# Kernel tuning notes

Measured on AMD Instinct MI355X. Metric: run time of the kernel, lower is better.

The kernel has to match this reference:

```python
import jax, jax.numpy as jnp
import numpy as np

NODELEN = 394
N_NODES = 50000
N_EDGES = 200000
IN_DIM = 2 * NODELEN  # 788
H2 = 192
EMB = 128


def setup_inputs() -> dict:
    key = jax.random.key(0)
    ks = jax.random.split(key, 12)
    inp = {
        'features': jax.random.normal(ks[0], (N_NODES, NODELEN), dtype=jnp.float32),
        'src': jax.random.randint(ks[1], (N_EDGES,), 0, N_NODES),
        'dst': jax.random.randint(ks[2], (N_EDGES,), 0, N_NODES),
        # AutoEncoder params (Linear weights stored as [in, out])
        'W_enc1': jax.random.normal(ks[3], (IN_DIM, H2), dtype=jnp.float32) / np.sqrt(IN_DIM),
        'b_enc1': jnp.zeros((H2,), dtype=jnp.float32),
        'W_enc3': jax.random.normal(ks[4], (H2, EMB), dtype=jnp.float32) / np.sqrt(H2),
        'b_enc3': jnp.zeros((EMB,), dtype=jnp.float32),
        'W_dec1': jax.random.normal(ks[5], (EMB, H2), dtype=jnp.float32) / np.sqrt(EMB),
        'b_dec1': jnp.zeros((H2,), dtype=jnp.float32),
        'W_dec3': jax.random.normal(ks[6], (H2, IN_DIM), dtype=jnp.float32) / np.sqrt(H2),
        'b_dec3': jnp.zeros((IN_DIM,), dtype=jnp.float32),
    }
    return inp


def _segment_mean(msgs, dst, inv_deg, n):
    # msgs: [E, F] gathered neighbor features; mean over incoming edges per node
    return jax.ops.segment_sum(msgs, dst, num_segments=n) * inv_deg


def reference(features, src, dst, W_enc1, b_enc1, W_enc3, b_enc3,
              W_dec1, b_dec1, W_dec3, b_dec3):
    n = features.shape[0]
    ones = jnp.ones(src.shape[0], dtype=features.dtype)
    deg = jax.ops.segment_sum(ones, dst, num_segments=n)
    # nodes with no neighbors fall back to the zero dummy vector (as in source)
    inv_deg = (1.0 / jnp.maximum(deg, 1.0))[:, None]

    # depth-1 aggregation: mean of raw neighbor features, then feat[0] := 0
    h1 = _segment_mean(features[src], dst, inv_deg, n)
    h1 = h1.at[:, 0].set(0.0)
    # depth-2 aggregation: mean of depth-1 aggregates of neighbors, feat[0] := 0
    h2 = _segment_mean(h1[src], dst, inv_deg, n)
    h2 = h2.at[:, 0].set(0.0)

    # concatenated embedding with positions 0 and NODELEN zeroed
    emb = jnp.concatenate([features, h2], axis=1)  # [N, 788]
    emb = emb.at[:, 0].set(0.0).at[:, NODELEN].set(0.0)

    # AutoEncoder forward (dropout is identity at inference)
    x = jax.nn.relu(emb @ W_enc1 + b_enc1)
    encoded = x @ W_enc3 + b_enc3
    y = jax.nn.relu(encoded @ W_dec1 + b_dec1)
    decoded = y @ W_dec3 + b_dec3
    return encoded, decoded, emb
```

## Files before the change

### kernel.cpp

```cpp
#include <hip/hip_runtime.h>
#include <hip/hip_bf16.h>

#define NODELEN 394
#define IN_DIM 788
#define H2DIM 192
#define EMBDIM 128
#define NCHUNK 197

typedef __attribute__((ext_vector_type(4))) float f32x4;
typedef __attribute__((ext_vector_type(8))) short bfrag;

static __device__ __forceinline__ unsigned short f2bf(float f) {
    union { float f; unsigned u; } v; v.f = f;
    unsigned r = v.u + 0x7FFFu + ((v.u >> 16) & 1u);
    return (unsigned short)(r >> 16);
}
static __device__ __forceinline__ float bf2f(unsigned short h) {
    union { unsigned u; float f; } v; v.u = ((unsigned)h) << 16;
    return v.f;
}


__global__ void count_deg(const int* __restrict__ dst, int* __restrict__ deg, int e) {
    int i = blockIdx.x * blockDim.x + threadIdx.x;
    if (i < e) atomicAdd(&deg[dst[i]], 1);
}

__global__ void block_sum(const int* __restrict__ deg, int* __restrict__ bsum, int n) {
    __shared__ int s[256];
    int t = threadIdx.x;
    int i = blockIdx.x * 256 + t;
    s[t] = (i < n) ? deg[i] : 0;
    __syncthreads();
    for (int d = 128; d > 0; d >>= 1) {
        if (t < d) s[t] += s[t + d];
        __syncthreads();
    }
    if (t == 0) bsum[blockIdx.x] = s[0];
}

__global__ void scan_bsums(int* bsum, int nb) {
    __shared__ int s[256];
    int t = threadIdx.x;
    int x0 = (t < nb) ? bsum[t] : 0;
    s[t] = x0;
    __syncthreads();
    for (int d = 1; d < 256; d <<= 1) {
        int u = (t >= d) ? s[t - d] : 0;
        __syncthreads();
        s[t] += u;
        __syncthreads();
    }
    if (t < nb) bsum[t] = s[t] - x0;
}

__global__ void block_scan(const int* __restrict__ deg, const int* __restrict__ boff,
                           int* __restrict__ rowstart, int* __restrict__ cursor,
                           float* __restrict__ inv, int n) {
    __shared__ int s[256];
    int t = threadIdx.x;
    int i = blockIdx.x * 256 + t;
    int x0 = (i < n) ? deg[i] : 0;
    s[t] = x0;
    __syncthreads();
    for (int d = 1; d < 256; d <<= 1) {
        int u = (t >= d) ? s[t - d] : 0;
        __syncthreads();
        s[t] += u;
        __syncthreads();
    }
    if (i < n) {
        int r = boff[blockIdx.x] + s[t] - x0;
        rowstart[i] = r;
        cursor[i] = r;
        inv[i] = 1.0f / fmaxf((float)x0, 1.0f);
    }
}

__global__ void fill_edges(const int* __restrict__ src, const int* __restrict__ dst,
                           int* __restrict__ cursor, int* __restrict__ elist, int e) {
    int i = blockIdx.x * blockDim.x + threadIdx.x;
    if (i < e) {
        int p = atomicAdd(&cursor[dst[i]], 1);
        elist[p] = src[i];
    }
}


__global__ __launch_bounds__(256) void gather1(
        const float* __restrict__ feat, const int* __restrict__ rowstart,
        const int* __restrict__ deg, const float* __restrict__ inv,
        const int* __restrict__ elist, unsigned short* __restrict__ h1) {
    const int node = blockIdx.x;
    const int c = threadIdx.x;
    if (c >= NCHUNK) return;
    const int beg = rowstart[node];
    const int dc = deg[node];
    const float s = inv[node];
    const size_t off = (size_t)c * 2;

    float ax = 0.f, ay = 0.f, bx = 0.f, by = 0.f;
    float cx = 0.f, cy = 0.f, dx = 0.f, dy = 0.f;
    int j = 0;
    for (; j + 3 < dc; j += 4) {
        int n0 = elist[beg + j], n1 = elist[beg + j + 1];
        int n2 = elist[beg + j + 2], n3 = elist[beg + j + 3];
        float2 v0 = *(const float2*)(feat + (size_t)n0 * NODELEN + off);
        float2 v1 = *(const float2*)(feat + (size_t)n1 * NODELEN + off);
        float2 v2 = *(const float2*)(feat + (size_t)n2 * NODELEN + off);
        float2 v3 = *(const float2*)(feat + (size_t)n3 * NODELEN + off);
        ax += v0.x; ay += v0.y; bx += v1.x; by += v1.y;
        cx += v2.x; cy += v2.y; dx += v3.x; dy += v3.y;
    }
    for (; j < dc; ++j) {
        int n0 = elist[beg + j];
        float2 v0 = *(const float2*)(feat + (size_t)n0 * NODELEN + off);
        ax += v0.x; ay += v0.y;
    }
    float fx = (ax + bx + cx + dx) * s;
    float fy = (ay + by + cy + dy) * s;
    if (c == 0) fx = 0.f;
    unsigned out = ((unsigned)f2bf(fy) << 16) | (unsigned)f2bf(fx);
    *(unsigned*)(h1 + (size_t)node * NODELEN + off) = out;
}

__global__ __launch_bounds__(256) void gather2_emb(
        const float* __restrict__ feat, const unsigned* __restrict__ h1,
        const int* __restrict__ rowstart, const int* __restrict__ deg,
        const float* __restrict__ inv, const int* __restrict__ elist,
        float* __restrict__ emb) {
    const int node = blockIdx.x;
    const int c = threadIdx.x;
    if (c >= NCHUNK) return;
    const int beg = rowstart[node];
    const int dc = deg[node];
    const float s = inv[node];

    float ax = 0.f, ay = 0.f, bx = 0.f, by = 0.f;
    float cx = 0.f, cy = 0.f, dx = 0.f, dy = 0.f;
    int j = 0;
    for (; j + 3 < dc; j += 4) {
        int n0 = elist[beg + j], n1 = elist[beg + j + 1];
        int n2 = elist[beg + j + 2], n3 = elist[beg + j + 3];
        unsigned u0 = h1[(size_t)n0 * NCHUNK + c];
        unsigned u1 = h1[(size_t)n1 * NCHUNK + c];
        unsigned u2 = h1[(size_t)n2 * NCHUNK + c];
        unsigned u3 = h1[(size_t)n3 * NCHUNK + c];
        ax += bf2f((unsigned short)u0); ay += bf2f((unsigned short)(u0 >> 16));
        bx += bf2f((unsigned short)u1); by += bf2f((unsigned short)(u1 >> 16));
        cx += bf2f((unsigned short)u2); cy += bf2f((unsigned short)(u2 >> 16));
        dx += bf2f((unsigned short)u3); dy += bf2f((unsigned short)(u3 >> 16));
    }
    for (; j < dc; ++j) {
        int n0 = elist[beg + j];
        unsigned u0 = h1[(size_t)n0 * NCHUNK + c];
        ax += bf2f((unsigned short)u0); ay += bf2f((unsigned short)(u0 >> 16));
    }
    float hx = (ax + bx + cx + dx) * s;
    float hy = (ay + by + cy + dy) * s;

    const float* fr = feat + (size_t)node * NODELEN;
    float* er = emb + (size_t)node * IN_DIM;
    float2 fv = *(const float2*)(fr + c * 2);
    if (c == 0) { fv.x = 0.f; hx = 0.f; }
    *(float2*)(er + c * 2) = fv;
    float2 hv; hv.x = hx; hv.y = hy;
    *(float2*)(er + NODELEN + c * 2) = hv;
}

__device__ __forceinline__ void tr_one(const float* W, unsigned short* Wt,
                                       int K, int N, int Kp, int idx) {
    int nrow = idx / Kp, k = idx - nrow * Kp;
    Wt[idx] = (k < K) ? f2bf(W[(size_t)k * N + nrow]) : (unsigned short)0;
}

#define T1E (192 * 800)
#define T2E (128 * 192)
#define T3E (192 * 128)
#define T4E (788 * 192)

__global__ void transpose_all(const float* __restrict__ W1, unsigned short* __restrict__ Wt1,
                              const float* __restrict__ W2, unsigned short* __restrict__ Wt2,
                              const float* __restrict__ W3, unsigned short* __restrict__ Wt3,
                              const float* __restrict__ W4, unsigned short* __restrict__ Wt4) {
    int idx = blockIdx.x * 256 + threadIdx.x;
    if (idx < T1E) { tr_one(W1, Wt1, IN_DIM, H2DIM, 800, idx); return; }
    idx -= T1E;
    if (idx < T2E) { tr_one(W2, Wt2, H2DIM, EMBDIM, 192, idx); return; }
    idx -= T2E;
    if (idx < T3E) { tr_one(W3, Wt3, EMBDIM, H2DIM, 128, idx); return; }
    idx -= T3E;
    if (idx < T4E) { tr_one(W4, Wt4, H2DIM, IN_DIM, 192, idx); return; }
}

__global__ __launch_bounds__(256) void mlp_fused(
    const float* __restrict__ emb,
    const unsigned short* __restrict__ Wt1,
    const unsigned short* __restrict__ Wt2,
    const unsigned short* __restrict__ Wt3,
    const unsigned short* __restrict__ Wt4,
    const float* __restrict__ b1, const float* __restrict__ b2,
    const float* __restrict__ b3, const float* __restrict__ b4,
    float* __restrict__ encoded, float* __restrict__ decoded, int M)
{
    __shared__ unsigned short As[64][40];
    __shared__ unsigned short Bs[192][40];
    __shared__ unsigned short XY[64][200];
    __shared__ unsigned short EN[64][136];

    const int tid = threadIdx.x;
    const int wid = tid >> 6, l = tid & 63;
    const int wm = wid >> 1, wn = wid & 1;
    const int lr = l & 15, lk = l >> 4;
    const int m0 = blockIdx.x * 64;

    {
        f32x4 acc[2][6];
        #pragma unroll
        for (int i = 0; i < 2; ++i)
            #pragma unroll
            for (int j = 0; j < 6; ++j) acc[i][j] = (f32x4){0.f, 0.f, 0.f, 0.f};

        for (int kt = 0; kt < 25; ++kt) {
            const int k0 = kt * 32;
            {
                int row = tid >> 2, q = tid & 3;
                int gm = m0 + row, gk = k0 + q * 8;
                float4 v0 = make_float4(0.f, 0.f, 0.f, 0.f);
                float4 v1 = make_float4(0.f, 0.f, 0.f, 0.f);
                if (gm < M) {
                    if (gk < IN_DIM)     v0 = *(const float4*)(emb + (size_t)gm * IN_DIM + gk);
                    if (gk + 4 < IN_DIM) v1 = *(const float4*)(emb + (size_t)gm * IN_DIM + gk + 4);
                }
                union { unsigned short u[8]; bfrag v; } pk;
                pk.u[0] = f2bf(v0.x); pk.u[1] = f2bf(v0.y);
                pk.u[2] = f2bf(v0.z); pk.u[3] = f2bf(v0.w);
                pk.u[4] = f2bf(v1.x); pk.u[5] = f2bf(v1.y);
                pk.u[6] = f2bf(v1.z); pk.u[7] = f2bf(v1.w);
                *(bfrag*)&As[row][q * 8] = pk.v;
            }
            for (int a = tid; a < 384; a += 256) {
                int row = a >> 1, h = a & 1;
                const unsigned short* p = Wt1 + (size_t)row * 800 + k0 + h * 16;
                *(bfrag*)&Bs[row][h * 16]     = *(const bfrag*)p;
                *(bfrag*)&Bs[row][h * 16 + 8] = *(const bfrag*)(p + 8);
            }
            __syncthreads();
            bfrag af[2], bf[6];
            #pragma unroll
            for (int i = 0; i < 2; ++i) af[i] = *(const bfrag*)&As[wm * 32 + i * 16 + lr][lk * 8];
            #pragma unroll
            for (int j = 0; j < 6; ++j) bf[j] = *(const bfrag*)&Bs[wn * 96 + j * 16 + lr][lk * 8];
            #pragma unroll
            for (int i = 0; i < 2; ++i)
                #pragma unroll
                for (int j = 0; j < 6; ++j)
                    acc[i][j] = __builtin_amdgcn_mfma_f32_16x16x32_bf16(af[i], bf[j], acc[i][j], 0, 0, 0);
            __syncthreads();
        }
        float bv[6];
        #pragma unroll
        for (int j = 0; j < 6; ++j) bv[j] = b1[wn * 96 + j * 16 + lr];
        #pragma unroll
        for (int i = 0; i < 2; ++i)
            #pragma unroll
            for (int j = 0; j < 6; ++j)
                #pragma unroll
                for (int r = 0; r < 4; ++r) {
                    int m = wm * 32 + i * 16 + lk * 4 + r;
                    int n1 = wn * 96 + j * 16 + lr;
                    XY[m][n1] = f2bf(fmaxf(acc[i][j][r] + bv[j], 0.f));
                }
        __syncthreads();
    }

    {
        f32x4 acc[2][4];
        #pragma unroll
        for (int i = 0; i < 2; ++i)
            #pragma unroll
            for (int j = 0; j < 4; ++j) acc[i][j] = (f32x4){0.f, 0.f, 0.f, 0.f};

        for (int kt = 0; kt < 6; ++kt) {
            const int k0 = kt * 32;
            {
                int row = tid >> 1, h = tid & 1;
                const unsigned short* p = Wt2 + (size_t)row * 192 + k0 + h * 16;
                *(bfrag*)&Bs[row][h * 16]     = *(const bfrag*)p;
                *(bfrag*)&Bs[row][h * 16 + 8] = *(const bfrag*)(p + 8);
            }
            __syncthreads();
            bfrag af[2], bf[4];
            #pragma unroll
            for (int i = 0; i < 2; ++i) af[i] = *(const bfrag*)&XY[wm * 32 + i * 16 + lr][k0 + lk * 8];
            #pragma unroll
            for (int j = 0; j < 4; ++j) bf[j] = *(const bfrag*)&Bs[wn * 64 + j * 16 + lr][lk * 8];
            #pragma unroll
            for (int i = 0; i < 2; ++i)
                #pragma unroll
                for (int j = 0; j < 4; ++j)
                    acc[i][j] = __builtin_amdgcn_mfma_f32_16x16x32_bf16(af[i], bf[j], acc[i][j], 0, 0, 0);
            __syncthreads();
        }
        float bv[4];
        #pragma unroll
        for (int j = 0; j < 4; ++j) bv[j] = b2[wn * 64 + j * 16 + lr];
        #pragma unroll
        for (int i = 0; i < 2; ++i)
            #pragma unroll
            for (int j = 0; j < 4; ++j)
                #pragma unroll
                for (int r = 0; r < 4; ++r) {
                    int m = wm * 32 + i * 16 + lk * 4 + r;
                    int n2 = wn * 64 + j * 16 + lr;
                    float v = acc[i][j][r] + bv[j];
                    int gm = m0 + m;
                    if (gm < M) encoded[(size_t)gm * EMBDIM + n2] = v;
                    EN[m][n2] = f2bf(v);
                }
        __syncthreads();
    }

    {
        f32x4 acc[2][6];
        #pragma unroll
        for (int i = 0; i < 2; ++i)
            #pragma unroll
            for (int j = 0; j < 6; ++j) acc[i][j] = (f32x4){0.f, 0.f, 0.f, 0.f};

        for (int kt = 0; kt < 4; ++kt) {
            const int k0 = kt * 32;
            for (int a = tid; a < 384; a += 256) {
                int row = a >> 1, h = a & 1;
                const unsigned short* p = Wt3 + (size_t)row * 128 + k0 + h * 16;
                *(bfrag*)&Bs[row][h * 16]     = *(const bfrag*)p;
                *(bfrag*)&Bs[row][h * 16 + 8] = *(const bfrag*)(p + 8);
            }
            __syncthreads();
            bfrag af[2], bf[6];
            #pragma unroll
            for (int i = 0; i < 2; ++i) af[i] = *(const bfrag*)&EN[wm * 32 + i * 16 + lr][k0 + lk * 8];
            #pragma unroll
            for (int j = 0; j < 6; ++j) bf[j] = *(const bfrag*)&Bs[wn * 96 + j * 16 + lr][lk * 8];
            #pragma unroll
            for (int i = 0; i < 2; ++i)
                #pragma unroll
                for (int j = 0; j < 6; ++j)
                    acc[i][j] = __builtin_amdgcn_mfma_f32_16x16x32_bf16(af[i], bf[j], acc[i][j], 0, 0, 0);
            __syncthreads();
        }
        float bv[6];
        #pragma unroll
        for (int j = 0; j < 6; ++j) bv[j] = b3[wn * 96 + j * 16 + lr];
        #pragma unroll
        for (int i = 0; i < 2; ++i)
            #pragma unroll
            for (int j = 0; j < 6; ++j)
                #pragma unroll
                for (int r = 0; r < 4; ++r) {
                    int m = wm * 32 + i * 16 + lk * 4 + r;
                    int n3 = wn * 96 + j * 16 + lr;
                    XY[m][n3] = f2bf(fmaxf(acc[i][j][r] + bv[j], 0.f));
                }
        __syncthreads();
    }

    for (int nc = 0; nc < 7; ++nc) {
        f32x4 acc[2][4];
        #pragma unroll
        for (int i = 0; i < 2; ++i)
            #pragma unroll
            for (int j = 0; j < 4; ++j) acc[i][j] = (f32x4){0.f, 0.f, 0.f, 0.f};

        for (int kt = 0; kt < 6; ++kt) {
            const int k0 = kt * 32;
            {
                int row = tid >> 1, h = tid & 1;
                int gn = nc * 128 + row;
                bfrag v0 = {0,0,0,0,0,0,0,0}, v1 = {0,0,0,0,0,0,0,0};
                if (gn < IN_DIM) {
                    const unsigned short* p = Wt4 + (size_t)gn * 192 + k0 + h * 16;
                    v0 = *(const bfrag*)p;
                    v1 = *(const bfrag*)(p + 8);
                }
                *(bfrag*)&Bs[row][h * 16]     = v0;
                *(bfrag*)&Bs[row][h * 16 + 8] = v1;
            }
            __syncthreads();
            bfrag af[2], bf[4];
            #pragma unroll
            for (int i = 0; i < 2; ++i) af[i] = *(const bfrag*)&XY[wm * 32 + i * 16 + lr][k0 + lk * 8];
            #pragma unroll
            for (int j = 0; j < 4; ++j) bf[j] = *(const bfrag*)&Bs[wn * 64 + j * 16 + lr][lk * 8];
            #pragma unroll
            for (int i = 0; i < 2; ++i)
                #pragma unroll
                for (int j = 0; j < 4; ++j)
                    acc[i][j] = __builtin_amdgcn_mfma_f32_16x16x32_bf16(af[i], bf[j], acc[i][j], 0, 0, 0);
            __syncthreads();
        }
        float bv[4];
        #pragma unroll
        for (int j = 0; j < 4; ++j) {
            int n4 = nc * 128 + wn * 64 + j * 16 + lr;
            bv[j] = (n4 < IN_DIM) ? b4[n4] : 0.f;
        }
        #pragma unroll
        for (int i = 0; i < 2; ++i)
            #pragma unroll
            for (int j = 0; j < 4; ++j)
                #pragma unroll
                for (int r = 0; r < 4; ++r) {
                    int m = wm * 32 + i * 16 + lk * 4 + r;
                    int n4 = nc * 128 + wn * 64 + j * 16 + lr;
                    int gm = m0 + m;
                    if (gm < M && n4 < IN_DIM)
                        decoded[(size_t)gm * IN_DIM + n4] = acc[i][j][r] + bv[j];
                }
    }
}


extern "C" void kernel_launch(void* const* d_in, const int* in_sizes, int n_in,
                              void* d_out, int out_size, void* d_ws, size_t ws_size,
                              hipStream_t stream) {
    const float* features = (const float*)d_in[0];
    const int*   src      = (const int*)d_in[1];
    const int*   dst      = (const int*)d_in[2];
    const float* W_enc1   = (const float*)d_in[3];
    const float* b_enc1   = (const float*)d_in[4];
    const float* W_enc3   = (const float*)d_in[5];
    const float* b_enc3   = (const float*)d_in[6];
    const float* W_dec1   = (const float*)d_in[7];
    const float* b_dec1   = (const float*)d_in[8];
    const float* W_dec3   = (const float*)d_in[9];
    const float* b_dec3   = (const float*)d_in[10];

    const int n = in_sizes[0] / NODELEN;
    const int e = in_sizes[1];

    float* encoded = (float*)d_out;
    float* decoded = encoded + (size_t)n * EMBDIM;
    float* emb     = decoded + (size_t)n * IN_DIM;

    char* ws = (char*)d_ws;
    unsigned short* h1  = (unsigned short*)(ws + 0);
    unsigned short* Wt1 = (unsigned short*)(ws + 40000000);
    unsigned short* Wt2 = (unsigned short*)(ws + 40400000);
    unsigned short* Wt3 = (unsigned short*)(ws + 40500000);
    unsigned short* Wt4 = (unsigned short*)(ws + 40600000);
    float* inv          = (float*)(ws + 41000000);
    int*   deg          = (int*)  (ws + 41200000);
    int*   rowstart     = (int*)  (ws + 41400000);
    int*   cursor       = (int*)  (ws + 41600000);
    int*   elist        = (int*)  (ws + 41800000);
    int*   bsum         = (int*)  (ws + 42600000);

    const int nb = (n + 255) / 256;
    const int eb = (e + 255) / 256;

    transpose_all<<<(T1E + T2E + T3E + T4E + 255) / 256, 256, 0, stream>>>(
        W_enc1, Wt1, W_enc3, Wt2, W_dec1, Wt3, W_dec3, Wt4);

    hipMemsetAsync(deg, 0, (size_t)n * sizeof(int), stream);
    count_deg<<<eb, 256, 0, stream>>>(dst, deg, e);
    block_sum<<<nb, 256, 0, stream>>>(deg, bsum, n);
    scan_bsums<<<1, 256, 0, stream>>>(bsum, nb);
    block_scan<<<nb, 256, 0, stream>>>(deg, bsum, rowstart, cursor, inv, n);
    fill_edges<<<eb, 256, 0, stream>>>(src, dst, cursor, elist, e);

    gather1<<<n, 256, 0, stream>>>(features, rowstart, deg, inv, elist, h1);
    gather2_emb<<<n, 256, 0, stream>>>(features, (const unsigned*)h1, rowstart, deg,
                                       inv, elist, emb);

    const int MB = (n + 63) / 64;
    mlp_fused<<<MB, 256, 0, stream>>>(emb, Wt1, Wt2, Wt3, Wt4,
                                      b_enc1, b_enc3, b_dec1, b_dec3,
                                      encoded, decoded, n);
}
```

Measured before the change: 387.7 us.

## Software-pipeline weight/activation loads in fused MLP and swizzle LDS layouts

Restructures the fused four-layer MLP kernel so global loads for the next K-tile (and the first tile of the next layer) are issued into registers while the current tile is consumed. The A operand of layer 1 is loaded straight into registers in MFMA fragment layout, which removes the As shared buffer. Padded LDS arrays become XOR-swizzled flat layouts to avoid bank conflicts, and the last layer caches its A fragments in registers across output chunks. It also switches to the library bf16 conversion and adds an occupancy hint. In exchange it uses more registers and more complex indexing, so spilling or lower occupancy are possible.

```diff
diff --git a/kernel.cpp b/kernel.cpp
--- a/kernel.cpp
+++ b/kernel.cpp
@@ -193,7 +193,58 @@
     if (idx < T4E) { tr_one(W4, Wt4, H2DIM, IN_DIM, 192, idx); return; }
 }
 
-__global__ __launch_bounds__(256) void mlp_fused(
+static __device__ __forceinline__ int bs_addr(int r, int s) {
+    return r * 32 + ((s ^ ((r >> 1) & 3)) << 3);
+}
+static __device__ __forceinline__ int xy_base(int r, int s) {
+    int ph = (s & 24) | ((s ^ r) & 7);
+    return r * 192 + (ph << 3);
+}
+static __device__ __forceinline__ int xy_addr_s(int r, int col) { return xy_base(r, col >> 3) + (col & 7); }
+static __device__ __forceinline__ int en_base(int r, int s) {
+    int ph = (s & 8) | ((s ^ r) & 7);
+    return r * 128 + (ph << 3);
+}
+static __device__ __forceinline__ int en_addr_s(int r, int col) { return en_base(r, col >> 3) + (col & 7); }
+
+static __device__ __forceinline__ unsigned short f2bf_fast(float f) {
+    __hip_bfloat16 h = __float2bfloat16(f);
+    union { __hip_bfloat16 h; unsigned short u; } c; c.h = h; return c.u;
+}
+
+struct A8 { float4 a, b; };
+
+static __device__ __forceinline__ void load_a(A8 out[2], const float* __restrict__ emb,
+                                              int m0, int wm, int lr, int lk, int M, int kt) {
+    int c = kt * 32 + lk * 8;
+    #pragma unroll
+    for (int i = 0; i < 2; ++i) {
+        int gm = m0 + wm * 32 + i * 16 + lr;
+        const float* rp = emb + (size_t)gm * IN_DIM;
+        bool v = gm < M;
+        if (v && c + 8 <= IN_DIM) {
+            out[i].a = *(const float4*)(rp + c);
+            out[i].b = *(const float4*)(rp + c + 4);
+        } else {
+            float t[8];
+            #pragma unroll
+            for (int q = 0; q < 8; ++q) t[q] = (v && c + q < IN_DIM) ? rp[c + q] : 0.f;
+            out[i].a = make_float4(t[0], t[1], t[2], t[3]);
+            out[i].b = make_float4(t[4], t[5], t[6], t[7]);
+        }
+    }
+}
+
+static __device__ __forceinline__ bfrag cvt_a(const A8& x) {
+    union { unsigned short u[8]; bfrag v; } pk;
+    pk.u[0] = f2bf_fast(x.a.x); pk.u[1] = f2bf_fast(x.a.y);
+    pk.u[2] = f2bf_fast(x.a.z); pk.u[3] = f2bf_fast(x.a.w);
+    pk.u[4] = f2bf_fast(x.b.x); pk.u[5] = f2bf_fast(x.b.y);
+    pk.u[6] = f2bf_fast(x.b.z); pk.u[7] = f2bf_fast(x.b.w);
+    return pk.v;
+}
+
+__global__ __launch_bounds__(256, 3) void mlp_fused(
     const float* __restrict__ emb,
     const unsigned short* __restrict__ Wt1,
     const unsigned short* __restrict__ Wt2,
@@ -203,61 +254,72 @@
     const float* __restrict__ b3, const float* __restrict__ b4,
     float* __restrict__ encoded, float* __restrict__ decoded, int M)
 {
-    __shared__ unsigned short As[64][40];
-    __shared__ unsigned short Bs[192][40];
-    __shared__ unsigned short XY[64][200];
-    __shared__ unsigned short EN[64][136];
+    __shared__ unsigned short Bs[192 * 32];
+    __shared__ unsigned short XY[64 * 192];
+    __shared__ unsigned short EN[64 * 128];
 
     const int tid = threadIdx.x;
     const int wid = tid >> 6, l = tid & 63;
     const int wm = wid >> 1, wn = wid & 1;
     const int lr = l & 15, lk = l >> 4;
     const int m0 = blockIdx.x * 64;
+    const bfrag zf = {0, 0, 0, 0, 0, 0, 0, 0};
+
+    const int r0 = tid >> 2, s0 = tid & 3;
+    const int r1 = (tid + 256) >> 2;
+    const int r2 = (tid + 512) >> 2;
+    const int bw0 = bs_addr(r0, s0);
+    const int bw1 = bs_addr(r1, s0);
+    const int bw2 = bs_addr(r2, s0);
+    int brd6[6], brd4[4];
+    #pragma unroll
+    for (int j = 0; j < 6; ++j) brd6[j] = bs_addr(wn * 96 + j * 16 + lr, lk);
+    #pragma unroll
+    for (int j = 0; j < 4; ++j) brd4[j] = bs_addr(wn * 64 + j * 16 + lr, lk);
 
     {
-        f32x4 acc[2][6];
+        f32x4 acc1[2][6];
         #pragma unroll
         for (int i = 0; i < 2; ++i)
             #pragma unroll
-            for (int j = 0; j < 6; ++j) acc[i][j] = (f32x4){0.f, 0.f, 0.f, 0.f};
-
+            for (int j = 0; j < 6; ++j) acc1[i][j] = (f32x4){0.f, 0.f, 0.f, 0.f};
+
+        A8 aC[2], aN[2];
+        bfrag bC[3], bN[3];
+        load_a(aC, emb, m0, wm, lr, lk, M, 0);
+        bC[0] = *(const bfrag*)(Wt1 + (size_t)r0 * 800 + s0 * 8);
+        bC[1] = *(const bfrag*)(Wt1 + (size_t)r1 * 800 + s0 * 8);
+        bC[2] = *(const bfrag*)(Wt1 + (size_t)r2 * 800 + s0 * 8);
+
+        #pragma unroll 5
         for (int kt = 0; kt < 25; ++kt) {
-            const int k0 = kt * 32;
-            {
-                int row = tid >> 2, q = tid & 3;
-                int gm = m0 + row, gk = k0 + q * 8;
-                float4 v0 = make_float4(0.f, 0.f, 0.f, 0.f);
-                float4 v1 = make_float4(0.f, 0.f, 0.f, 0.f);
-                if (gm < M) {
-                    if (gk < IN_DIM)     v0 = *(const float4*)(emb + (size_t)gm * IN_DIM + gk);
-                    if (gk + 4 < IN_DIM) v1 = *(const float4*)(emb + (size_t)gm * IN_DIM + gk + 4);
-                }
-                union { unsigned short u[8]; bfrag v; } pk;
-                pk.u[0] = f2bf(v0.x); pk.u[1] = f2bf(v0.y);
-                pk.u[2] = f2bf(v0.z); pk.u[3] = f2bf(v0.w);
-                pk.u[4] = f2bf(v1.x); pk.u[5] = f2bf(v1.y);
-                pk.u[6] = f2bf(v1.z); pk.u[7] = f2bf(v1.w);
-                *(bfrag*)&As[row][q * 8] = pk.v;
-            }
-            for (int a = tid; a < 384; a += 256) {
-                int row = a >> 1, h = a & 1;
-                const unsigned short* p = Wt1 + (size_t)row * 800 + k0 + h * 16;
-                *(bfrag*)&Bs[row][h * 16]     = *(const bfrag*)p;
-                *(bfrag*)&Bs[row][h * 16 + 8] = *(const bfrag*)(p + 8);
+            *(bfrag*)&Bs[bw0] = bC[0];
+            *(bfrag*)&Bs[bw1] = bC[1];
+            *(bfrag*)&Bs[bw2] = bC[2];
+            if (kt < 24) {
+                int k0 = (kt + 1) * 32;
+                load_a(aN, emb, m0, wm, lr, lk, M, kt + 1);
+                bN[0] = *(const bfrag*)(Wt1 + (size_t)r0 * 800 + k0 + s0 * 8);
+                bN[1] = *(const bfrag*)(Wt1 + (size_t)r1 * 800 + k0 + s0 * 8);
+                bN[2] = *(const bfrag*)(Wt1 + (size_t)r2 * 800 + k0 + s0 * 8);
             }
             __syncthreads();
-            bfrag af[2], bf[6];
-            #pragma unroll
-            for (int i = 0; i < 2; ++i) af[i] = *(const bfrag*)&As[wm * 32 + i * 16 + lr][lk * 8];
-            #pragma unroll
-            for (int j = 0; j < 6; ++j) bf[j] = *(const bfrag*)&Bs[wn * 96 + j * 16 + lr][lk * 8];
-            #pragma unroll
-            for (int i = 0; i < 2; ++i)
-                #pragma unroll
-                for (int j = 0; j < 6; ++j)
-                    acc[i][j] = __builtin_amdgcn_mfma_f32_16x16x32_bf16(af[i], bf[j], acc[i][j], 0, 0, 0);
+            bfrag af0 = cvt_a(aC[0]), af1 = cvt_a(aC[1]);
+            bfrag bf[6];
+            #pragma unroll
+            for (int j = 0; j < 6; ++j) bf[j] = *(const bfrag*)&Bs[brd6[j]];
+            #pragma unroll
+            for (int j = 0; j < 6; ++j) {
+                acc1[0][j] = __builtin_amdgcn_mfma_f32_16x16x32_bf16(af0, bf[j], acc1[0][j], 0, 0, 0);
+                acc1[1][j] = __builtin_amdgcn_mfma_f32_16x16x32_bf16(af1, bf[j], acc1[1][j], 0, 0, 0);
+            }
             __syncthreads();
+            if (kt < 24) {
+                aC[0] = aN[0]; aC[1] = aN[1];
+                bC[0] = bN[0]; bC[1] = bN[1]; bC[2] = bN[2];
+            }
         }
+
         float bv[6];
         #pragma unroll
         for (int j = 0; j < 6; ++j) bv[j] = b1[wn * 96 + j * 16 + lr];
@@ -269,39 +331,51 @@
                 for (int r = 0; r < 4; ++r) {
                     int m = wm * 32 + i * 16 + lk * 4 + r;
                     int n1 = wn * 96 + j * 16 + lr;
-                    XY[m][n1] = f2bf(fmaxf(acc[i][j][r] + bv[j], 0.f));
+                    XY[xy_addr_s(m, n1)] = f2bf_fast(fmaxf(acc1[i][j][r] + bv[j], 0.f));
                 }
-        __syncthreads();
-    }
-
+    }
+
+    bfrag c3[3], n3[3];
     {
-        f32x4 acc[2][4];
+        bfrag c2[2], n2[2];
+        c2[0] = *(const bfrag*)(Wt2 + (size_t)r0 * 192 + s0 * 8);
+        c2[1] = *(const bfrag*)(Wt2 + (size_t)r1 * 192 + s0 * 8);
+        f32x4 acc2[2][4];
         #pragma unroll
         for (int i = 0; i < 2; ++i)
             #pragma unroll
-            for (int j = 0; j < 4; ++j) acc[i][j] = (f32x4){0.f, 0.f, 0.f, 0.f};
-
+            for (int j = 0; j < 4; ++j) acc2[i][j] = (f32x4){0.f, 0.f, 0.f, 0.f};
+
+        #pragma unroll
         for (int kt = 0; kt < 6; ++kt) {
-            const int k0 = kt * 32;
-            {
-                int row = tid >> 1, h = tid & 1;
-                const unsigned short* p = Wt2 + (size_t)row * 192 + k0 + h * 16;
-                *(bfrag*)&Bs[row][h * 16]     = *(const bfrag*)p;
-                *(bfrag*)&Bs[row][h * 16 + 8] = *(const bfrag*)(p + 8);
+            *(bfrag*)&Bs[bw0] = c2[0];
+            *(bfrag*)&Bs[bw1] = c2[1];
+            if (kt < 5) {
+                int k0 = (kt + 1) * 32;
+                n2[0] = *(const bfrag*)(Wt2 + (size_t)r0 * 192 + k0 + s0 * 8);
+                n2[1] = *(const bfrag*)(Wt2 + (size_t)r1 * 192 + k0 + s0 * 8);
+            } else {
+                c3[0] = *(const bfrag*)(Wt3 + (size_t)r0 * 128 + s0 * 8);
+                c3[1] = *(const bfrag*)(Wt3 + (size_t)r1 * 128 + s0 * 8);
+                c3[2] = *(const bfrag*)(Wt3 + (size_t)r2 * 128 + s0 * 8);
             }
             __syncthreads();
-            bfrag af[2], bf[4];
-            #pragma unroll
-            for (int i = 0; i < 2; ++i) af[i] = *(const bfrag*)&XY[wm * 32 + i * 16 + lr][k0 + lk * 8];
-            #pragma unroll
-            for (int j = 0; j < 4; ++j) bf[j] = *(const bfrag*)&Bs[wn * 64 + j * 16 + lr][lk * 8];
+            bfrag af[2];
             #pragma unroll
             for (int i = 0; i < 2; ++i)
+                af[i] = *(const bfrag*)&XY[xy_base(wm * 32 + i * 16 + lr, kt * 4 + lk)];
+            bfrag bf[4];
+            #pragma unroll
+            for (int j = 0; j < 4; ++j) bf[j] = *(const bfrag*)&Bs[brd4[j]];
+            #pragma unroll
+            for (int i = 0; i < 2; ++i)
                 #pragma unroll
                 for (int j = 0; j < 4; ++j)
-                    acc[i][j] = __builtin_amdgcn_mfma_f32_16x16x32_bf16(af[i], bf[j], acc[i][j], 0, 0, 0);
+                    acc2[i][j] = __builtin_amdgcn_mfma_f32_16x16x32_bf16(af[i], bf[j], acc2[i][j], 0, 0, 0);
             __syncthreads();
+            if (kt < 5) { c2[0] = n2[0]; c2[1] = n2[1]; }
         }
+
         float bv[4];
         #pragma unroll
         for (int j = 0; j < 4; ++j) bv[j] = b2[wn * 64 + j * 16 + lr];
@@ -312,43 +386,53 @@
                 #pragma unroll
                 for (int r = 0; r < 4; ++r) {
                     int m = wm * 32 + i * 16 + lk * 4 + r;
-                    int n2 = wn * 64 + j * 16 + lr;
-                    float v = acc[i][j][r] + bv[j];
+                    int nn = wn * 64 + j * 16 + lr;
+                    float v = acc2[i][j][r] + bv[j];
                     int gm = m0 + m;
-                    if (gm < M) encoded[(size_t)gm * EMBDIM + n2] = v;
-                    EN[m][n2] = f2bf(v);
+                    if (gm < M) encoded[(size_t)gm * EMBDIM + nn] = v;
+                    EN[en_addr_s(m, nn)] = f2bf_fast(v);
                 }
-        __syncthreads();
-    }
-
+    }
+
+    bfrag c4[2], n4[2];
     {
-        f32x4 acc[2][6];
+        f32x4 acc3[2][6];
         #pragma unroll
         for (int i = 0; i < 2; ++i)
             #pragma unroll
-            for (int j = 0; j < 6; ++j) acc[i][j] = (f32x4){0.f, 0.f, 0.f, 0.f};
-
+            for (int j = 0; j < 6; ++j) acc3[i][j] = (f32x4){0.f, 0.f, 0.f, 0.f};
+
+        #pragma unroll
         for (int kt = 0; kt < 4; ++kt) {
-            const int k0 = kt * 32;
-            for (int a = tid; a < 384; a += 256) {
-                int row = a >> 1, h = a & 1;
-                const unsigned short* p = Wt3 + (size_t)row * 128 + k0 + h * 16;
-                *(bfrag*)&Bs[row][h * 16]     = *(const bfrag*)p;
-                *(bfrag*)&Bs[row][h * 16 + 8] = *(const bfrag*)(p + 8);
+            *(bfrag*)&Bs[bw0] = c3[0];
+            *(bfrag*)&Bs[bw1] = c3[1];
+            *(bfrag*)&Bs[bw2] = c3[2];
+            if (kt < 3) {
+                int k0 = (kt + 1) * 32;
+                n3[0] = *(const bfrag*)(Wt3 + (size_t)r0 * 128 + k0 + s0 * 8);
+                n3[1] = *(const bfrag*)(Wt3 + (size_t)r1 * 128 + k0 + s0 * 8);
+                n3[2] = *(const bfrag*)(Wt3 + (size_t)r2 * 128 + k0 + s0 * 8);
+            } else {
+                c4[0] = *(const bfrag*)(Wt4 + (size_t)r0 * 192 + s0 * 8);
+                c4[1] = *(const bfrag*)(Wt4 + (size_t)r1 * 192 + s0 * 8);
             }
             __syncthreads();
-            bfrag af[2], bf[6];
-            #pragma unroll
-            for (int i = 0; i < 2; ++i) af[i] = *(const bfrag*)&EN[wm * 32 + i * 16 + lr][k0 + lk * 8];
-            #pragma unroll
-            for (int j = 0; j < 6; ++j) bf[j] = *(const bfrag*)&Bs[wn * 96 + j * 16 + lr][lk * 8];
+            bfrag af[2];
             #pragma unroll
             for (int i = 0; i < 2; ++i)
+                af[i] = *(const bfrag*)&EN[en_base(wm * 32 + i * 16 + lr, kt * 4 + lk)];
+            bfrag bf[6];
+            #pragma unroll
+            for (int j = 0; j < 6; ++j) bf[j] = *(const bfrag*)&Bs[brd6[j]];
+            #pragma unroll
+            for (int i = 0; i < 2; ++i)
                 #pragma unroll
                 for (int j = 0; j < 6; ++j)
-                    acc[i][j] = __builtin_amdgcn_mfma_f32_16x16x32_bf16(af[i], bf[j], acc[i][j], 0, 0, 0);
+                    acc3[i][j] = __builtin_amdgcn_mfma_f32_16x16x32_bf16(af[i], bf[j], acc3[i][j], 0, 0, 0);
             __syncthreads();
+            if (kt < 3) { c3[0] = n3[0]; c3[1] = n3[1]; c3[2] = n3[2]; }
         }
+
         float bv[6];
         #pragma unroll
         for (int j = 0; j < 6; ++j) bv[j] = b3[wn * 96 + j * 16 + lr];
@@ -359,64 +443,71 @@
                 #pragma unroll
                 for (int r = 0; r < 4; ++r) {
                     int m = wm * 32 + i * 16 + lk * 4 + r;
-                    int n3 = wn * 96 + j * 16 + lr;
-                    XY[m][n3] = f2bf(fmaxf(acc[i][j][r] + bv[j], 0.f));
+                    int n3c = wn * 96 + j * 16 + lr;
+                    XY[xy_addr_s(m, n3c)] = f2bf_fast(fmaxf(acc3[i][j][r] + bv[j], 0.f));
                 }
-        __syncthreads();
-    }
-
-    for (int nc = 0; nc < 7; ++nc) {
-        f32x4 acc[2][4];
-        #pragma unroll
-        for (int i = 0; i < 2; ++i)
-            #pragma unroll
-            for (int j = 0; j < 4; ++j) acc[i][j] = (f32x4){0.f, 0.f, 0.f, 0.f};
-
-        for (int kt = 0; kt < 6; ++kt) {
-            const int k0 = kt * 32;
-            {
-                int row = tid >> 1, h = tid & 1;
-                int gn = nc * 128 + row;
-                bfrag v0 = {0,0,0,0,0,0,0,0}, v1 = {0,0,0,0,0,0,0,0};
-                if (gn < IN_DIM) {
-                    const unsigned short* p = Wt4 + (size_t)gn * 192 + k0 + h * 16;
-                    v0 = *(const bfrag*)p;
-                    v1 = *(const bfrag*)(p + 8);
+    }
+
+    {
+        bfrag af4[6][2];
+        for (int nc = 0; nc < 7; ++nc) {
+            f32x4 acc4[2][4];
+            #pragma unroll
+            for (int i = 0; i < 2; ++i)
+                #pragma unroll
+                for (int j = 0; j < 4; ++j) acc4[i][j] = (f32x4){0.f, 0.f, 0.f, 0.f};
+
+            #pragma unroll
+            for (int kt = 0; kt < 6; ++kt) {
+                *(bfrag*)&Bs[bw0] = c4[0];
+                *(bfrag*)&Bs[bw1] = c4[1];
+                {
+                    int nn = (kt < 5) ? nc : nc + 1;
+                    int nk = (kt < 5) ? (kt + 1) * 32 : 0;
+                    if (nn < 7) {
+                        int g0 = nn * 128 + r0, g1 = nn * 128 + r1;
+                        n4[0] = (g0 < IN_DIM) ? *(const bfrag*)(Wt4 + (size_t)g0 * 192 + nk + s0 * 8) : zf;
+                        n4[1] = (g1 < IN_DIM) ? *(const bfrag*)(Wt4 + (size_t)g1 * 192 + nk + s0 * 8) : zf;
+                    }
                 }
-                *(bfrag*)&Bs[row][h * 16]     = v0;
-                *(bfrag*)&Bs[row][h * 16 + 8] = v1;
-            }
-            __syncthreads();
-            bfrag af[2], bf[4];
-            #pragma unroll
-            for (int i = 0; i < 2; ++i) af[i] = *(const bfrag*)&XY[wm * 32 + i * 16 + lr][k0 + lk * 8];
-            #pragma unroll
-            for (int j = 0; j < 4; ++j) bf[j] = *(const bfrag*)&Bs[wn * 64 + j * 16 + lr][lk * 8];
+                __syncthreads();
+                if (nc == 0 && kt == 0) {
+                    #pragma unroll
+                    for (int q = 0; q < 6; ++q)
+                        #pragma unroll
+                        for (int i = 0; i < 2; ++i)
+                            af4[q][i] = *(const bfrag*)&XY[xy_base(wm * 32 + i * 16 + lr, q * 4 + lk)];
+                }
+                bfrag bf[4];
+                #pragma unroll
+                for (int j = 0; j < 4; ++j) bf[j] = *(const bfrag*)&Bs[brd4[j]];
+                #pragma unroll
+                for (int i = 0; i < 2; ++i)
+                    #pragma unroll
+                    for (int j = 0; j < 4; ++j)
+                        acc4[i][j] = __builtin_amdgcn_mfma_f32_16x16x32_bf16(af4[kt][i], bf[j], acc4[i][j], 0, 0, 0);
+                __syncthreads();
+                c4[0] = n4[0]; c4[1] = n4[1];
+            }
+
+            float bv[4];
+            #pragma unroll
+            for (int j = 0; j < 4; ++j) {
+                int nn = nc * 128 + wn * 64 + j * 16 + lr;
+                bv[j] = (nn < IN_DIM) ? b4[nn] : 0.f;
+            }
             #pragma unroll
             for (int i = 0; i < 2; ++i)
                 #pragma unroll
                 for (int j = 0; j < 4; ++j)
-                    acc[i][j] = __builtin_amdgcn_mfma_f32_16x16x32_bf16(af[i], bf[j], acc[i][j], 0, 0, 0);
-            __syncthreads();
+                    #pragma unroll
+                    for (int r = 0; r < 4; ++r) {
+                        int gm = m0 + wm * 32 + i * 16 + lk * 4 + r;
+                        int nn = nc * 128 + wn * 64 + j * 16 + lr;
+                        if (gm < M && nn < IN_DIM)
+                            decoded[(size_t)gm * IN_DIM + nn] = acc4[i][j][r] + bv[j];
+                    }
         }
-        float bv[4];
-        #pragma unroll
-        for (int j = 0; j < 4; ++j) {
-            int n4 = nc * 128 + wn * 64 + j * 16 + lr;
-            bv[j] = (n4 < IN_DIM) ? b4[n4] : 0.f;
-        }
-        #pragma unroll
-        for (int i = 0; i < 2; ++i)
-            #pragma unroll
-            for (int j = 0; j < 4; ++j)
-                #pragma unroll
-                for (int r = 0; r < 4; ++r) {
-                    int m = wm * 32 + i * 16 + lk * 4 + r;
-                    int n4 = nc * 128 + wn * 64 + j * 16 + lr;
-                    int gm = m0 + m;
-                    if (gm < M && n4 < IN_DIM)
-                        decoded[(size_t)gm * IN_DIM + n4] = acc[i][j][r] + bv[j];
-                }
     }
 }
 
```

New measurement: 353.1 us. 8.9% less time.
